# Kernel optimization log

Measured on AMD Instinct MI355X. Metric: run time of the kernel, lower is better.

Reference implementation:

```python
import jax, jax.numpy as jnp
import numpy as np

B = 262144
NUM_CLASSES = 1000
K = 4
CODE_DIM = 256


def setup_inputs() -> dict:
    key = jax.random.key(0)
    k1, k2, k3 = jax.random.split(key, 3)
    codes = jax.random.uniform(k1, (B, CODE_DIM), dtype=jnp.float32)
    pred_class = jax.random.randint(k2, (B,), 0, NUM_CLASSES, dtype=jnp.int64)
    centroids = jax.random.uniform(k3, (NUM_CLASSES, K, CODE_DIM), dtype=jnp.float32)
    return {"codes": codes, "pred_class": pred_class, "centroids": centroids}


def reference(codes, pred_class, centroids):
    # Gather the k centroids of each sample's predicted class: [B, K, D]
    cents = centroids[pred_class]
    # Mean absolute (normalized Hamming-style) distance per centroid: [B, K]
    d = jnp.mean(jnp.abs(codes[:, None, :] - cents), axis=2)
    # Min over the k centroids -> [B]
    return jnp.min(d, axis=1)
```

## Files before the change

kernel.cpp:

```cpp
#include <hip/hip_runtime.h>


#define B_TOTAL     262144
#define NUM_CLASSES 1000
#define KC          4
#define DIM         256
#define SPW         8

typedef float    vf4 __attribute__((ext_vector_type(4)));
typedef _Float16 vh4 __attribute__((ext_vector_type(4)));

__global__ __launch_bounds__(256) void convert_kernel(
    const float* __restrict__ cent_f32, _Float16* __restrict__ cent_f16)
{
    const int i = blockIdx.x * 256 + threadIdx.x;
    const int n = NUM_CLASSES * KC * DIM / 4;
    if (i < n) {
        const vf4 v = ((const vf4*)cent_f32)[i];
        vh4 h;
        h.x = (_Float16)v.x; h.y = (_Float16)v.y;
        h.z = (_Float16)v.z; h.w = (_Float16)v.w;
        ((vh4*)cent_f16)[i] = h;
    }
}

__global__ __launch_bounds__(256) void sparse_codebook_w(
    const float*    __restrict__ codes,
    const int*      __restrict__ pred_class,
    const _Float16* __restrict__ cent_f16,
    float*          __restrict__ out)
{
    const int wave = (blockIdx.x * 256 + threadIdx.x) >> 6;
    const int lane = threadIdx.x & 63;
    const int s0   = wave * SPW;
    if (s0 >= B_TOTAL) return;

    int cls[SPW];
#pragma unroll
    for (int s = 0; s < SPW; ++s)
        cls[s] = pred_class[s0 + s];

    const vf4* cv = (const vf4*)codes;

    vf4 c_next = __builtin_nontemporal_load(&cv[(size_t)s0 * 64 + lane]);

#pragma unroll
    for (int s = 0; s < SPW; ++s) {
        const vf4 c = c_next;
        if (s + 1 < SPW)
            c_next = __builtin_nontemporal_load(
                &cv[(size_t)(s0 + s + 1) * 64 + lane]);

        const vh4* cb = (const vh4*)cent_f16
                      + (size_t)cls[s] * (KC * DIM / 4) + lane;
        const vh4 g0 = cb[0];
        const vh4 g1 = cb[64];
        const vh4 g2 = cb[128];
        const vh4 g3 = cb[192];

        float d0 = fabsf(c.x - (float)g0.x) + fabsf(c.y - (float)g0.y)
                 + fabsf(c.z - (float)g0.z) + fabsf(c.w - (float)g0.w);
        float d1 = fabsf(c.x - (float)g1.x) + fabsf(c.y - (float)g1.y)
                 + fabsf(c.z - (float)g1.z) + fabsf(c.w - (float)g1.w);
        float d2 = fabsf(c.x - (float)g2.x) + fabsf(c.y - (float)g2.y)
                 + fabsf(c.z - (float)g2.z) + fabsf(c.w - (float)g2.w);
        float d3 = fabsf(c.x - (float)g3.x) + fabsf(c.y - (float)g3.y)
                 + fabsf(c.z - (float)g3.z) + fabsf(c.w - (float)g3.w);

        const bool b0 = (lane & 1) != 0;
        const bool b1 = (lane & 2) != 0;
        float ka = b0 ? d1 : d0;
        float kb = b0 ? d0 : d1;
        ka += __shfl_xor(kb, 1, 64);
        float kc = b0 ? d3 : d2;
        float kd = b0 ? d2 : d3;
        kc += __shfl_xor(kd, 1, 64);
        float ke = b1 ? kc : ka;
        float kf = b1 ? ka : kc;
        ke += __shfl_xor(kf, 2, 64);
        ke += __shfl_xor(ke, 4, 64);
        ke += __shfl_xor(ke, 8, 64);
        ke += __shfl_xor(ke, 16, 64);
        ke += __shfl_xor(ke, 32, 64);
        float m = fminf(ke, __shfl_xor(ke, 1, 64));
        m = fminf(m, __shfl_xor(m, 2, 64));

        if (lane == 0)
            __builtin_nontemporal_store(m * (1.0f / (float)DIM),
                                        &out[s0 + s]);
    }
}

extern "C" void kernel_launch(void* const* d_in, const int* in_sizes, int n_in,
                              void* d_out, int out_size, void* d_ws, size_t ws_size,
                              hipStream_t stream) {
    const float* codes = (const float*)d_in[0];
    const int*   pred  = (const int*)d_in[1];
    const float* cents = (const float*)d_in[2];
    float*       out   = (float*)d_out;
    _Float16*    tab   = (_Float16*)d_ws;

    const int nvec = NUM_CLASSES * KC * DIM / 4;
    convert_kernel<<<(nvec + 255) / 256, 256, 0, stream>>>(cents, tab);

    const int waves  = B_TOTAL / SPW;
    const int blocks = (waves * 64) / 256;
    sparse_codebook_w<<<blocks, 256, 0, stream>>>(codes, pred, tab, out);
}
```

Baseline: 369.9 us.

## Counting-sort samples by class so waves reuse centroid loads

Adds a histogram, a prefix scan and a scatter pass that bucket sample indices by predicted class. The main kernel then walks the sorted list, reloading the four centroids only when the class changes, while codes are gathered by index and outputs scattered. This is meant to cut centroid gather traffic, at the cost of three extra kernel launches, global atomics, and non-contiguous row accesses to codes.

```diff
diff --git a/kernel.cpp b/kernel.cpp
--- a/kernel.cpp
+++ b/kernel.cpp
@@ -9,6 +9,11 @@
 
 typedef float    vf4 __attribute__((ext_vector_type(4)));
 typedef _Float16 vh4 __attribute__((ext_vector_type(4)));
+
+#define WS_TAB_OFF   0
+#define WS_HIST_OFF  2097152
+#define WS_OFFS_OFF  (2097152 + 4096)
+#define WS_SORT_OFF  (2097152 + 8192)
 
 __global__ __launch_bounds__(256) void convert_kernel(
     const float* __restrict__ cent_f32, _Float16* __restrict__ cent_f16)
@@ -24,39 +29,87 @@
     }
 }
 
-__global__ __launch_bounds__(256) void sparse_codebook_w(
+__global__ __launch_bounds__(256) void hist_kernel(
+    const int* __restrict__ pred, int* __restrict__ hist)
+{
+    __shared__ int lh[NUM_CLASSES];
+    for (int c = threadIdx.x; c < NUM_CLASSES; c += 256) lh[c] = 0;
+    __syncthreads();
+    const int i = blockIdx.x * 256 + threadIdx.x;
+    atomicAdd(&lh[pred[i]], 1);
+    __syncthreads();
+    for (int c = threadIdx.x; c < NUM_CLASSES; c += 256) {
+        const int v = lh[c];
+        if (v) atomicAdd(&hist[c], v);
+    }
+}
+
+__global__ __launch_bounds__(1024) void scan_kernel(
+    const int* __restrict__ hist, int* __restrict__ offs)
+{
+    __shared__ int sh[1024];
+    const int t = threadIdx.x;
+    const int h = (t < NUM_CLASSES) ? hist[t] : 0;
+    sh[t] = h;
+    __syncthreads();
+    for (int off = 1; off < 1024; off <<= 1) {
+        const int v = (t >= off) ? sh[t - off] : 0;
+        __syncthreads();
+        sh[t] += v;
+        __syncthreads();
+    }
+    if (t < NUM_CLASSES) offs[t] = sh[t] - h;
+}
+
+__global__ __launch_bounds__(256) void scatter_kernel(
+    const int* __restrict__ pred, int* __restrict__ offs,
+    unsigned* __restrict__ sorted)
+{
+    const int i = blockIdx.x * 256 + threadIdx.x;
+    const int c = pred[i];
+    const int r = atomicAdd(&offs[c], 1);
+    sorted[r] = (unsigned)i | ((unsigned)c << 18);
+}
+
+__global__ __launch_bounds__(256) void sparse_codebook_s(
     const float*    __restrict__ codes,
-    const int*      __restrict__ pred_class,
+    const unsigned* __restrict__ sorted,
     const _Float16* __restrict__ cent_f16,
     float*          __restrict__ out)
 {
     const int wave = (blockIdx.x * 256 + threadIdx.x) >> 6;
     const int lane = threadIdx.x & 63;
     const int s0   = wave * SPW;
-    if (s0 >= B_TOTAL) return;
 
-    int cls[SPW];
+    unsigned e[SPW];
 #pragma unroll
     for (int s = 0; s < SPW; ++s)
-        cls[s] = pred_class[s0 + s];
+        e[s] = sorted[s0 + s];
 
     const vf4* cv = (const vf4*)codes;
+    vf4 c_next = __builtin_nontemporal_load(
+        &cv[(size_t)(e[0] & 0x3FFFFu) * 64 + lane]);
 
-    vf4 c_next = __builtin_nontemporal_load(&cv[(size_t)s0 * 64 + lane]);
+    int cur_cls = -1;
+    vh4 g0, g1, g2, g3;
 
 #pragma unroll
     for (int s = 0; s < SPW; ++s) {
         const vf4 c = c_next;
         if (s + 1 < SPW)
             c_next = __builtin_nontemporal_load(
-                &cv[(size_t)(s0 + s + 1) * 64 + lane]);
+                &cv[(size_t)(e[s + 1] & 0x3FFFFu) * 64 + lane]);
 
-        const vh4* cb = (const vh4*)cent_f16
-                      + (size_t)cls[s] * (KC * DIM / 4) + lane;
-        const vh4 g0 = cb[0];
-        const vh4 g1 = cb[64];
-        const vh4 g2 = cb[128];
-        const vh4 g3 = cb[192];
+        const int cls = (int)(e[s] >> 18);
+        if (cls != cur_cls) {
+            const vh4* cb = (const vh4*)cent_f16
+                          + (size_t)cls * (KC * DIM / 4) + lane;
+            g0 = cb[0];
+            g1 = cb[64];
+            g2 = cb[128];
+            g3 = cb[192];
+            cur_cls = cls;
+        }
 
         float d0 = fabsf(c.x - (float)g0.x) + fabsf(c.y - (float)g0.y)
                  + fabsf(c.z - (float)g0.z) + fabsf(c.w - (float)g0.w);
@@ -87,7 +140,7 @@
 
         if (lane == 0)
             __builtin_nontemporal_store(m * (1.0f / (float)DIM),
-                                        &out[s0 + s]);
+                                        &out[e[s] & 0x3FFFFu]);
     }
 }
 
@@ -98,12 +151,23 @@
     const int*   pred  = (const int*)d_in[1];
     const float* cents = (const float*)d_in[2];
     float*       out   = (float*)d_out;
-    _Float16*    tab   = (_Float16*)d_ws;
+
+    char*      ws     = (char*)d_ws;
+    _Float16*  tab    = (_Float16*)(ws + WS_TAB_OFF);
+    int*       hist   = (int*)(ws + WS_HIST_OFF);
+    int*       offs   = (int*)(ws + WS_OFFS_OFF);
+    unsigned*  sorted = (unsigned*)(ws + WS_SORT_OFF);
+
+    hipMemsetAsync(hist, 0, 4096, stream);
 
     const int nvec = NUM_CLASSES * KC * DIM / 4;
     convert_kernel<<<(nvec + 255) / 256, 256, 0, stream>>>(cents, tab);
 
+    hist_kernel<<<B_TOTAL / 256, 256, 0, stream>>>(pred, hist);
+    scan_kernel<<<1, 1024, 0, stream>>>(hist, offs);
+    scatter_kernel<<<B_TOTAL / 256, 256, 0, stream>>>(pred, offs, sorted);
+
     const int waves  = B_TOTAL / SPW;
     const int blocks = (waves * 64) / 256;
-    sparse_codebook_w<<<blocks, 256, 0, stream>>>(codes, pred, tab, out);
+    sparse_codebook_s<<<blocks, 256, 0, stream>>>(codes, sorted, tab, out);
 }
```

After: 433.5 us. +17.2%, slower.
